# Kernel optimization log

Hardware: AMD Instinct MI355X
Metric: run time of the kernel (lower is better)

Reference implementation:

```python
import jax, jax.numpy as jnp
import numpy as np

B, N, IN_DIM, SLOT_DIM, HIDDEN = 32, 4096, 256, 256, 512
NUM_SLOTS, NUM_ITERS = 8, 3
EPS_LN = 1e-5


def layernorm(x, g, b):
    m = jnp.mean(x, axis=-1, keepdims=True)
    v = jnp.var(x, axis=-1, keepdims=True)
    return (x - m) * jax.lax.rsqrt(v + EPS_LN) * g + b


def setup_inputs() -> dict:
    key = jax.random.key(0)
    ks = jax.random.split(key, 16)
    s = 0.02
    return {
        "inputs": jax.random.normal(ks[0], (B, N, IN_DIM), jnp.float32),
        "init_noise": jax.random.normal(ks[1], (B, NUM_SLOTS, SLOT_DIM), jnp.float32),
        "mu": jax.random.normal(ks[2], (1, 1, SLOT_DIM), jnp.float32),
        "sigma_raw": jax.random.normal(ks[3], (1, 1, SLOT_DIM), jnp.float32),
        "ln_in_g": jnp.ones((IN_DIM,), jnp.float32), "ln_in_b": jnp.zeros((IN_DIM,), jnp.float32),
        "ln_s_g": jnp.ones((SLOT_DIM,), jnp.float32), "ln_s_b": jnp.zeros((SLOT_DIM,), jnp.float32),
        "ln_m_g": jnp.ones((SLOT_DIM,), jnp.float32), "ln_m_b": jnp.zeros((SLOT_DIM,), jnp.float32),
        "wq": jax.random.normal(ks[4], (SLOT_DIM, SLOT_DIM), jnp.float32) * s,
        "bq": jnp.zeros((SLOT_DIM,), jnp.float32),
        "wk": jax.random.normal(ks[5], (SLOT_DIM, IN_DIM), jnp.float32) * s,
        "bk": jnp.zeros((SLOT_DIM,), jnp.float32),
        "wv": jax.random.normal(ks[6], (SLOT_DIM, IN_DIM), jnp.float32) * s,
        "bv": jnp.zeros((SLOT_DIM,), jnp.float32),
        "w_ih": jax.random.normal(ks[7], (3 * SLOT_DIM, SLOT_DIM), jnp.float32) * s,
        "w_hh": jax.random.normal(ks[8], (3 * SLOT_DIM, SLOT_DIM), jnp.float32) * s,
        "b_ih": jnp.zeros((3 * SLOT_DIM,), jnp.float32),
        "b_hh": jnp.zeros((3 * SLOT_DIM,), jnp.float32),
        "w1": jax.random.normal(ks[9], (HIDDEN, SLOT_DIM), jnp.float32) * s,
        "b1": jnp.zeros((HIDDEN,), jnp.float32),
        "w2": jax.random.normal(ks[10], (SLOT_DIM, HIDDEN), jnp.float32) * s,
        "b2": jnp.zeros((SLOT_DIM,), jnp.float32),
    }


def gru_cell(x, h, w_ih, w_hh, b_ih, b_hh):
    # PyTorch GRUCell: gates split as (reset, update, new)
    gx = x @ w_ih.T + b_ih
    gh = h @ w_hh.T + b_hh
    xr, xz, xn = jnp.split(gx, 3, axis=-1)
    hr, hz, hn = jnp.split(gh, 3, axis=-1)
    r = jax.nn.sigmoid(xr + hr)
    z = jax.nn.sigmoid(xz + hz)
    n = jnp.tanh(xn + r * hn)
    return (1.0 - z) * n + z * h


def reference(inputs, init_noise, mu, sigma_raw, ln_in_g, ln_in_b, ln_s_g, ln_s_b,
              ln_m_g, ln_m_b, wq, bq, wk, bk, wv, bv, w_ih, w_hh, b_ih, b_hh,
              w1, b1, w2, b2):
    scale = SLOT_DIM ** (-0.5)
    x = layernorm(inputs, ln_in_g, ln_in_b)          # [B,N,Din]
    k = x @ wk.T + bk                                # [B,N,D]
    v = x @ wv.T + bv                                # [B,N,D]
    sigma = jax.nn.softplus(sigma_raw)
    slots = mu + sigma * init_noise                  # [B,S,D]
    attn = None
    for _ in range(NUM_ITERS):
        slots_prev = slots
        q = layernorm(slots, ln_s_g, ln_s_b) @ wq.T + bq      # [B,S,D]
        logits = jnp.einsum('bnd,bsd->bns', k, q) * scale     # [B,N,S]
        attn = jax.nn.softmax(logits, axis=-1) + 1e-8         # softmax over slots
        attn = attn / jnp.sum(attn, axis=1, keepdims=True)    # renorm over inputs
        updates = jnp.einsum('bnd,bns->bsd', v, attn)         # [B,S,D]
        slots = gru_cell(updates, slots_prev, w_ih, w_hh, b_ih, b_hh)
        h = jax.nn.relu(layernorm(slots, ln_m_g, ln_m_b) @ w1.T + b1)
        slots = slots + (h @ w2.T + b2)
    return slots, attn
```

## Files before the change

kernel.cpp:

```cpp
#include <hip/hip_runtime.h>
#include <hip/hip_fp16.h>
#include <cstdint>

#define DEV static __device__ __forceinline__

typedef _Float16 f16x2 __attribute__((ext_vector_type(2)));

DEV float fdot2u(uint32_t a, uint32_t b, float c){
  union U { uint32_t u; f16x2 h; };
  U ua; ua.u = a; U ub; ub.u = b;
#if __has_builtin(__builtin_amdgcn_fdot2)
  return __builtin_amdgcn_fdot2(ua.h, ub.h, c, false);
#else
  return c + (float)ua.h[0]*(float)ub.h[0] + (float)ua.h[1]*(float)ub.h[1];
#endif
}

DEV float dot4(uint4 x, uint4 w, float a){
  a = fdot2u(x.x, w.x, a); a = fdot2u(x.y, w.y, a);
  a = fdot2u(x.z, w.z, a); a = fdot2u(x.w, w.w, a);
  return a;
}

DEV float wsum64(float v){
  #pragma unroll
  for (int o = 32; o; o >>= 1) v += __shfl_xor(v, o);
  return v;
}

DEV uint32_t pack2h(float a, float b){
  __half ha = __float2half(a), hb = __float2half(b);
  return (uint32_t)__half_as_ushort(ha) | ((uint32_t)__half_as_ushort(hb) << 16);
}

DEV uint32_t packsh(float v){
  float o = __shfl_xor(v, 1);
  return pack2h(v, o);
}

DEV uint4 packrow8(const float* p){
  uint4 r;
  r.x = pack2h(p[0], p[1]); r.y = pack2h(p[2], p[3]);
  r.z = pack2h(p[4], p[5]); r.w = pack2h(p[6], p[7]);
  return r;
}

__global__ __launch_bounds__(256) void k_tr(
  const float* __restrict__ wq, const float* __restrict__ wv,
  const float* __restrict__ wih, const float* __restrict__ whh,
  const float* __restrict__ w1, const float* __restrict__ w2,
  const float* __restrict__ wk,
  uint4* __restrict__ WQp4, uint4* __restrict__ WVp4,
  uint4* __restrict__ WIHp4, uint4* __restrict__ WHHp4,
  uint4* __restrict__ W1p4, uint4* __restrict__ W2p4,
  uint4* __restrict__ WKp4)
{
  int u = blockIdx.x * 256 + threadIdx.x;
  if (u < 8192){
    int e4 = u >> 8, n = u & 255;
    WVp4[u] = packrow8(wv + n*256 + 8*e4);
  } else if (u < 32768){
    int v = u - 8192; int e4 = v / 768, n = v - e4*768;
    WIHp4[v] = packrow8(wih + n*256 + 8*e4);
  } else if (u < 57344){
    int v = u - 32768; int e4 = v / 768, n = v - e4*768;
    WHHp4[v] = packrow8(whh + n*256 + 8*e4);
  } else if (u < 73728){
    int v = u - 57344; int e4 = v >> 9, n = v & 511;
    W1p4[v] = packrow8(w1 + n*256 + 8*e4);
  } else if (u < 90112){
    int v = u - 73728; int e4 = v >> 8, n = v & 255;
    W2p4[v] = packrow8(w2 + n*512 + 8*e4);
  } else if (u < 98304){
    int v = u - 90112; int e4 = v >> 8, n = v & 255;
    WQp4[v] = packrow8(wq + n*256 + 8*e4);
  } else if (u < 106496){
    int v = u - 98304; int d4 = v >> 8, c = v & 255;
    uint4 r;
    r.x = pack2h(wk[(8*d4+0)*256 + c], wk[(8*d4+1)*256 + c]);
    r.y = pack2h(wk[(8*d4+2)*256 + c], wk[(8*d4+3)*256 + c]);
    r.z = pack2h(wk[(8*d4+4)*256 + c], wk[(8*d4+5)*256 + c]);
    r.w = pack2h(wk[(8*d4+6)*256 + c], wk[(8*d4+7)*256 + c]);
    WKp4[v] = r;
  }
}

__global__ __launch_bounds__(256) void k_ln(
  const float* __restrict__ xin, const float* __restrict__ g,
  const float* __restrict__ b, uint32_t* __restrict__ xhat)
{
  int row = blockIdx.x * 4 + (threadIdx.x >> 6);
  int lane = threadIdx.x & 63;
  const float4 xv = ((const float4*)(xin + (size_t)row * 256))[lane];
  float s1 = wsum64(xv.x + xv.y + xv.z + xv.w);
  float s2 = wsum64(xv.x*xv.x + xv.y*xv.y + xv.z*xv.z + xv.w*xv.w);
  float m = s1 * (1.0f/256.0f);
  float var = s2 * (1.0f/256.0f) - m*m;
  float rstd = rsqrtf(var + 1e-5f);
  float4 gv = ((const float4*)g)[lane];
  float4 bv = ((const float4*)b)[lane];
  float y0 = (xv.x - m)*rstd*gv.x + bv.x;
  float y1 = (xv.y - m)*rstd*gv.y + bv.y;
  float y2 = (xv.z - m)*rstd*gv.z + bv.z;
  float y3 = (xv.w - m)*rstd*gv.w + bv.w;
  ((uint2*)(xhat + (size_t)row * 128))[lane] = make_uint2(pack2h(y0,y1), pack2h(y2,y3));
}

template<int MODE>
__global__ __launch_bounds__(512) void k_slot(
  const float* __restrict__ noise, const float* __restrict__ mu,
  const float* __restrict__ sigraw, float* __restrict__ S0,
  const float* __restrict__ uacc, const float* __restrict__ asum,
  const uint4* __restrict__ WVp4, const float* __restrict__ bv,
  const uint4* __restrict__ WIHp4, const uint4* __restrict__ WHHp4,
  const float* __restrict__ bih, const float* __restrict__ bhh,
  const float* __restrict__ lmg, const float* __restrict__ lmb,
  const uint4* __restrict__ W1p4, const float* __restrict__ b1,
  const uint4* __restrict__ W2p4, const float* __restrict__ b2,
  const float* __restrict__ lsg, const float* __restrict__ lsb,
  const uint4* __restrict__ WQp4, const float* __restrict__ bq,
  const uint4* __restrict__ WKp4, const float* __restrict__ bk,
  uint32_t* __restrict__ QTH, float* __restrict__ CV,
  float* __restrict__ uacc_z, float* __restrict__ asum_z)
{
  __shared__ float gx[768], gh[768];
  __shared__ float part[512];
  __shared__ uint4 hs4[32], un4[32], us4[32], sln4[32], q4[32];
  __shared__ uint4 hb4[64];
  __shared__ float redA[8], redB[8];

  const int t = threadIdx.x;
  const int h = t >> 8;
  const int c = t & 255;
  const int lane = t & 63;
  const int w8 = t >> 6;
  const int r = blockIdx.x;
  const int b = r >> 3, s = r & 7;

  float snv = 0.f, spv = 0.f;

  if (MODE == 0){
    if (t < 256){
      float x = sigraw[c];
      float sp = (x > 20.0f) ? x : log1pf(__expf(x));
      snv = mu[c] + sp * noise[r*256 + c];
      S0[r*256 + c] = snv;
    }
  } else {
    float ainv = 1.0f / asum[r];
    float hv = 0.f;
    if (t < 256){
      hv = S0[r*256 + c];
      float unv = uacc[r*256 + c] * ainv;
      uint32_t ph = packsh(hv), pu = packsh(unv);
      if (!(c & 1)){
        ((uint32_t*)hs4)[c>>1] = ph;
        ((uint32_t*)un4)[c>>1] = pu;
      }
    }
    __syncthreads();

    {
      float a = 0.f;
      #pragma unroll 8
      for (int e4 = h*16; e4 < h*16 + 16; ++e4)
        a = dot4(un4[e4], WVp4[e4*256 + c], a);
      part[t] = a;
    }
    __syncthreads();
    if (t < 256){
      float us = part[t] + part[t + 256] + bv[c];
      uint32_t p = packsh(us);
      if (!(c & 1)) ((uint32_t*)us4)[c>>1] = p;
    }
    __syncthreads();

    {
      const uint4* IN4 = h ? hs4 : us4;
      const uint4* WP = h ? WHHp4 : WIHp4;
      float a0 = 0.f, a1 = 0.f, a2 = 0.f;
      #pragma unroll 8
      for (int e4 = 0; e4 < 32; ++e4){
        uint4 x = IN4[e4];
        a0 = dot4(x, WP[e4*768 + c], a0);
        a1 = dot4(x, WP[e4*768 + 256 + c], a1);
        a2 = dot4(x, WP[e4*768 + 512 + c], a2);
      }
      float* OUT = h ? gh : gx;
      OUT[c] = a0; OUT[256 + c] = a1; OUT[512 + c] = a2;
    }
    __syncthreads();

    if (t < 256){
      float xr = gx[c]     + bih[c];
      float xz = gx[256+c] + bih[256+c];
      float xn = gx[512+c] + bih[512+c];
      float hr = gh[c]     + bhh[c];
      float hz = gh[256+c] + bhh[256+c];
      float hn = gh[512+c] + bhh[512+c];
      float rg = 1.f/(1.f + __expf(-(xr + hr)));
      float zg = 1.f/(1.f + __expf(-(xz + hz)));
      float ng = tanhf(xn + rg*hn);
      spv = (1.f - zg)*ng + zg*hv;
      float a = wsum64(spv), bs = wsum64(spv*spv);
      if (lane == 0){ redA[w8] = a; redB[w8] = bs; }
    }
    __syncthreads();
    {
      float s1 = redA[0]+redA[1]+redA[2]+redA[3];
      float s2 = redB[0]+redB[1]+redB[2]+redB[3];
      float m = s1*(1.f/256.f), var = s2*(1.f/256.f) - m*m;
      float rstd = rsqrtf(var + 1e-5f);
      if (t < 256){
        float slv = (spv - m)*rstd*lmg[c] + lmb[c];
        uint32_t p = packsh(slv);
        if (!(c & 1)) ((uint32_t*)sln4)[c>>1] = p;
      }
    }
    __syncthreads();

    {
      float a = 0.f;
      #pragma unroll 8
      for (int e4 = 0; e4 < 32; ++e4)
        a = dot4(sln4[e4], W1p4[e4*512 + t], a);
      float hval = fmaxf(a + b1[t], 0.f);
      float o = __shfl_xor(hval, 1);
      if (!(t & 1)) ((uint32_t*)hb4)[t>>1] = pack2h(hval, o);
    }
    __syncthreads();

    {
      float a = 0.f;
      #pragma unroll 8
      for (int e4 = h*32; e4 < h*32 + 32; ++e4)
        a = dot4(hb4[e4], W2p4[e4*256 + c], a);
      part[t] = a;
    }
    __syncthreads();
    if (t < 256){
      snv = spv + part[t] + part[t + 256] + b2[c];
      S0[r*256 + c] = snv;
    }
  }

  if (MODE != 2){
    if (t < 256){
      float a = wsum64(snv), bs = wsum64(snv*snv);
      if (lane == 0){ redA[w8] = a; redB[w8] = bs; }
    }
    __syncthreads();
    {
      float s1 = redA[0]+redA[1]+redA[2]+redA[3];
      float s2 = redB[0]+redB[1]+redB[2]+redB[3];
      float m = s1*(1.f/256.f), var = s2*(1.f/256.f) - m*m;
      float rstd = rsqrtf(var + 1e-5f);
      if (t < 256){
        float slv = (snv - m)*rstd*lsg[c] + lsb[c];
        uint32_t p = packsh(slv);
        if (!(c & 1)) ((uint32_t*)sln4)[c>>1] = p;
      }
    }
    __syncthreads();

    {
      float a = 0.f;
      #pragma unroll 8
      for (int e4 = h*16; e4 < h*16 + 16; ++e4)
        a = dot4(sln4[e4], WQp4[e4*256 + c], a);
      part[t] = a;
    }
    __syncthreads();
    if (t < 256){
      float qv = part[t] + part[t + 256] + bq[c];
      float p = wsum64(bk[c] * qv);
      if (lane == 0) redA[w8] = p;
      uint32_t pk = packsh(qv);
      if (!(c & 1)) ((uint32_t*)q4)[c>>1] = pk;
    }
    __syncthreads();
    {
      float cv = redA[0]+redA[1]+redA[2]+redA[3];
      if (t == 0) CV[r] = cv;
    }

    {
      float a = 0.f;
      #pragma unroll 8
      for (int e4 = h*16; e4 < h*16 + 16; ++e4)
        a = dot4(q4[e4], WKp4[e4*256 + c], a);
      part[t] = a;
    }
    __syncthreads();
    if (t < 256){
      float qtv = part[t] + part[t + 256];
      uint32_t p = packsh(qtv);
      if (!(c & 1)) QTH[b*1024 + (c>>1)*8 + s] = p;
      uacc_z[r*256 + c] = 0.f;
    }
    if (t == 0) asum_z[r] = 0.f;
  }
}

template<bool LAST>
__global__ __launch_bounds__(256) void k_attn(
  const uint32_t* __restrict__ xhat,
  const uint32_t* __restrict__ qtpk, const float* __restrict__ cvec,
  float* __restrict__ uacc, float* __restrict__ asum,
  float* __restrict__ attn_out)
{
  __shared__ uint32_t xs[64*135];
  __shared__ float lg[64*12];
  __shared__ uint32_t qs[1024];
  __shared__ float cs[8];
  const int b = blockIdx.y, chunk = blockIdx.x;
  const int t = threadIdx.x;
  const int lane = t & 63, w = t >> 6;
  for (int i = t; i < 1024; i += 256) qs[i] = qtpk[b*1024 + i];
  if (t < 8) cs[t] = cvec[b*8 + t];
  float up[8] = {0,0,0,0,0,0,0,0};
  float asl[8] = {0,0,0,0,0,0,0,0};
  const int shf = (t & 1) * 16;
  for (int st = 0; st < 4; ++st){
    const int gr0 = b*4096 + chunk*256 + st*64;
    __syncthreads();
    #pragma unroll
    for (int k = 0; k < 8; ++k){
      int c4 = k*256 + t;
      int row = c4 >> 5, j = c4 & 31;
      uint4 dv = ((const uint4*)xhat)[(size_t)(gr0 + row)*32 + j];
      uint32_t* dst = xs + row*135 + j*4;
      dst[0] = dv.x; dst[1] = dv.y; dst[2] = dv.z; dst[3] = dv.w;
    }
    __syncthreads();
    {
      const int s0 = w*2;
      float d0 = 0.f, d1 = 0.f;
      const uint32_t* xr = xs + lane*135;
      #pragma unroll
      for (int dp = 0; dp < 128; ++dp){
        uint32_t x = xr[dp];
        uint2 q = *(const uint2*)(qs + dp*8 + s0);
        d0 = fdot2u(x, q.x, d0);
        d1 = fdot2u(x, q.y, d1);
      }
      *(float2*)(lg + lane*12 + s0) = make_float2(d0, d1);
    }
    __syncthreads();
    if (t < 64){
      float l[8];
      float4 a = *(const float4*)(lg + t*12);
      float4 b4 = *(const float4*)(lg + t*12 + 4);
      l[0]=a.x; l[1]=a.y; l[2]=a.z; l[3]=a.w;
      l[4]=b4.x; l[5]=b4.y; l[6]=b4.z; l[7]=b4.w;
      #pragma unroll
      for (int s = 0; s < 8; ++s) l[s] = (l[s] + cs[s]) * 0.0625f;
      float mx = l[0];
      #pragma unroll
      for (int s = 1; s < 8; ++s) mx = fmaxf(mx, l[s]);
      float sum = 0.f;
      #pragma unroll
      for (int s = 0; s < 8; ++s){ l[s] = __expf(l[s] - mx); sum += l[s]; }
      float inv = 1.0f / sum;
      #pragma unroll
      for (int s = 0; s < 8; ++s){ l[s] = l[s]*inv + 1e-8f; asl[s] += l[s]; }
      float4 o0 = make_float4(l[0], l[1], l[2], l[3]);
      float4 o1 = make_float4(l[4], l[5], l[6], l[7]);
      *(float4*)(lg + t*12) = o0;
      *(float4*)(lg + t*12 + 4) = o1;
      if (LAST){
        float4* ap = (float4*)(attn_out + (size_t)(gr0 + t)*8);
        ap[0] = o0; ap[1] = o1;
      }
    }
    __syncthreads();
    {
      const uint32_t* xc = xs + (t >> 1);
      #pragma unroll 8
      for (int r = 0; r < 64; ++r){
        uint32_t u = xc[r*135];
        float x = __half2float(__ushort_as_half((unsigned short)(u >> shf)));
        float4 a0 = *(const float4*)(lg + r*12);
        float4 a1 = *(const float4*)(lg + r*12 + 4);
        up[0] += a0.x*x; up[1] += a0.y*x; up[2] += a0.z*x; up[3] += a0.w*x;
        up[4] += a1.x*x; up[5] += a1.y*x; up[6] += a1.z*x; up[7] += a1.w*x;
      }
    }
  }
  #pragma unroll
  for (int s = 0; s < 8; ++s) atomicAdd(&uacc[(b*8 + s)*256 + t], up[s]);
  if (t < 64){
    #pragma unroll
    for (int s = 0; s < 8; ++s){
      float v = wsum64(asl[s]);
      if (t == 0) atomicAdd(&asum[b*8 + s], v);
    }
  }
}

__global__ __launch_bounds__(256) void k_out(
  const float* __restrict__ S0, const float* __restrict__ asum,
  float* __restrict__ out)
{
  int i = blockIdx.x * 256 + threadIdx.x;
  if (i < 65536) out[i] = S0[i];
  else {
    int j = i - 65536;
    int b = j >> 15;
    int s = j & 7;
    out[i] = out[i] * (1.0f / asum[b*8 + s]);
  }
}

extern "C" void kernel_launch(void* const* d_in, const int* in_sizes, int n_in,
                              void* d_out, int out_size, void* d_ws, size_t ws_size,
                              hipStream_t stream) {
  const float* inputs = (const float*)d_in[0];
  const float* noise  = (const float*)d_in[1];
  const float* mu     = (const float*)d_in[2];
  const float* sigraw = (const float*)d_in[3];
  const float* lng    = (const float*)d_in[4];
  const float* lnb    = (const float*)d_in[5];
  const float* lsg    = (const float*)d_in[6];
  const float* lsb    = (const float*)d_in[7];
  const float* lmg    = (const float*)d_in[8];
  const float* lmb    = (const float*)d_in[9];
  const float* wq     = (const float*)d_in[10];
  const float* bq     = (const float*)d_in[11];
  const float* wk     = (const float*)d_in[12];
  const float* bk     = (const float*)d_in[13];
  const float* wv     = (const float*)d_in[14];
  const float* bv     = (const float*)d_in[15];
  const float* wih    = (const float*)d_in[16];
  const float* whh    = (const float*)d_in[17];
  const float* bih    = (const float*)d_in[18];
  const float* bhh    = (const float*)d_in[19];
  const float* w1     = (const float*)d_in[20];
  const float* b1     = (const float*)d_in[21];
  const float* w2     = (const float*)d_in[22];
  const float* b2     = (const float*)d_in[23];
  float* out = (float*)d_out;

  char* w = (char*)d_ws;
  size_t o = 0;
  uint32_t* XH = (uint32_t*)w;  o += 67108864;
  uint32_t* QT = (uint32_t*)(w + o); o += 131072;
  float* CV  = (float*)(w + o); o += 1024;
  float* UA  = (float*)(w + o); o += 262144;
  float* AS  = (float*)(w + o); o += 1024;
  float* S0  = (float*)(w + o); o += 262144;
  uint4* WQp = (uint4*)(w + o); o += 131072;
  uint4* WVp = (uint4*)(w + o); o += 131072;
  uint4* WIHp= (uint4*)(w + o); o += 393216;
  uint4* WHHp= (uint4*)(w + o); o += 393216;
  uint4* W1p = (uint4*)(w + o); o += 262144;
  uint4* W2p = (uint4*)(w + o); o += 262144;
  uint4* WKp = (uint4*)(w + o); o += 131072;

  k_tr<<<416, 256, 0, stream>>>(wq, wv, wih, whh, w1, w2, wk,
                                WQp, WVp, WIHp, WHHp, W1p, W2p, WKp);
  k_ln<<<32768, 256, 0, stream>>>(inputs, lng, lnb, XH);
  k_slot<0><<<256, 512, 0, stream>>>(noise, mu, sigraw, S0, UA, AS,
      WVp, bv, WIHp, WHHp, bih, bhh, lmg, lmb, W1p, b1, W2p, b2,
      lsg, lsb, WQp, bq, WKp, bk, QT, CV, UA, AS);

  dim3 ga(16, 32);
  for (int it = 0; it < 3; ++it){
    if (it == 2) k_attn<true ><<<ga, 256, 0, stream>>>(XH, QT, CV, UA, AS, out + 65536);
    else         k_attn<false><<<ga, 256, 0, stream>>>(XH, QT, CV, UA, AS, out + 65536);
    if (it < 2)
      k_slot<1><<<256, 512, 0, stream>>>(noise, mu, sigraw, S0, UA, AS,
          WVp, bv, WIHp, WHHp, bih, bhh, lmg, lmb, W1p, b1, W2p, b2,
          lsg, lsb, WQp, bq, WKp, bk, QT, CV, UA, AS);
    else
      k_slot<2><<<256, 512, 0, stream>>>(noise, mu, sigraw, S0, UA, AS,
          WVp, bv, WIHp, WHHp, bih, bhh, lmg, lmb, W1p, b1, W2p, b2,
          lsg, lsb, WQp, bq, WKp, bk, QT, CV, UA, AS);
  }
  k_out<<<4352, 256, 0, stream>>>(S0, AS, out);
}
```

Baseline: 429.9 us.

## Restructure attention kernel with MFMA logits, async LDS loads and swizzled layout

Rewrites k_attn so the k·q logits are computed with 16x16x32 f16 MFMA instead of per-lane fdot2 loops, and the softmax over slots runs in all waves using lane shuffles rather than a single wave. Input tiles are now copied straight from global memory into a XOR-swizzled LDS buffer with global_load_lds, which replaces the padded register-staged copy. Each wave now handles its own 16 rows for the update accumulation, and the partial sums are reduced in LDS before the atomics. This removes the serial softmax bottleneck and the scalar dot products, at the cost of more barriers and a cross-wave reduction at the end.

```diff
diff --git a/kernel.cpp b/kernel.cpp
--- a/kernel.cpp
+++ b/kernel.cpp
@@ -5,6 +5,8 @@
 #define DEV static __device__ __forceinline__
 
 typedef _Float16 f16x2 __attribute__((ext_vector_type(2)));
+typedef _Float16 f16x8 __attribute__((ext_vector_type(8)));
+typedef float    f32x4 __attribute__((ext_vector_type(4)));
 
 DEV float fdot2u(uint32_t a, uint32_t b, float c){
   union U { uint32_t u; f16x2 h; };
@@ -43,6 +45,12 @@
   r.x = pack2h(p[0], p[1]); r.y = pack2h(p[2], p[3]);
   r.z = pack2h(p[4], p[5]); r.w = pack2h(p[6], p[7]);
   return r;
+}
+
+DEV void gld16(const void* g, void* l){
+  __builtin_amdgcn_global_load_lds(
+      (const __attribute__((address_space(1))) void*)g,
+      (__attribute__((address_space(3))) void*)l, 16, 0, 0);
 }
 
 __global__ __launch_bounds__(256) void k_tr(
@@ -309,93 +317,134 @@
   float* __restrict__ uacc, float* __restrict__ asum,
   float* __restrict__ attn_out)
 {
-  __shared__ uint32_t xs[64*135];
-  __shared__ float lg[64*12];
+  __shared__ uint32_t xs[8192];
   __shared__ uint32_t qs[1024];
-  __shared__ float cs[8];
+  __shared__ float attn_lds[64][16];
+  __shared__ float up_lds[8][256];
+
   const int b = blockIdx.y, chunk = blockIdx.x;
   const int t = threadIdx.x;
-  const int lane = t & 63, w = t >> 6;
+  const int l = t & 63, w = t >> 6;
+  const int g = l >> 4, sl = l & 15;
+
   for (int i = t; i < 1024; i += 256) qs[i] = qtpk[b*1024 + i];
-  if (t < 8) cs[t] = cvec[b*8 + t];
-  float up[8] = {0,0,0,0,0,0,0,0};
-  float asl[8] = {0,0,0,0,0,0,0,0};
-  const int shf = (t & 1) * 16;
+
+  auto stage = [&](int st){
+    const size_t gr0 = (size_t)b*4096 + (size_t)chunk*256 + st*64;
+    #pragma unroll
+    for (int i = 0; i < 8; ++i){
+      int n  = w*8 + i;
+      int rl = 2*n + (l >> 5);
+      int ql = (l & 31) ^ (rl & 7);
+      gld16(xhat + (gr0 + rl)*128 + ql*4, xs + n*256);
+    }
+  };
+
+  stage(0);
+  __syncthreads();
+
+  uint4 bq[8];
+  #pragma unroll
+  for (int kk = 0; kk < 8; ++kk){
+    if (sl < 8){
+      uint4 v;
+      v.x = qs[(16*kk + 4*g + 0)*8 + sl];
+      v.y = qs[(16*kk + 4*g + 1)*8 + sl];
+      v.z = qs[(16*kk + 4*g + 2)*8 + sl];
+      v.w = qs[(16*kk + 4*g + 3)*8 + sl];
+      bq[kk] = v;
+    } else bq[kk] = make_uint4(0u,0u,0u,0u);
+  }
+  const float cv = (sl < 8) ? cvec[b*8 + sl] : 0.f;
+
+  float up[8][4];
+  #pragma unroll
+  for (int s = 0; s < 8; ++s){ up[s][0]=0.f; up[s][1]=0.f; up[s][2]=0.f; up[s][3]=0.f; }
+  float asl_acc = 0.f;
+
   for (int st = 0; st < 4; ++st){
-    const int gr0 = b*4096 + chunk*256 + st*64;
-    __syncthreads();
+    if (st){ __syncthreads(); stage(st); __syncthreads(); }
+    const int L0 = 16*w;
+
+    f32x4 acc; acc[0]=0.f; acc[1]=0.f; acc[2]=0.f; acc[3]=0.f;
+    const int rowA = L0 + sl;
     #pragma unroll
-    for (int k = 0; k < 8; ++k){
-      int c4 = k*256 + t;
-      int row = c4 >> 5, j = c4 & 31;
-      uint4 dv = ((const uint4*)xhat)[(size_t)(gr0 + row)*32 + j];
-      uint32_t* dst = xs + row*135 + j*4;
-      dst[0] = dv.x; dst[1] = dv.y; dst[2] = dv.z; dst[3] = dv.w;
-    }
-    __syncthreads();
-    {
-      const int s0 = w*2;
-      float d0 = 0.f, d1 = 0.f;
-      const uint32_t* xr = xs + lane*135;
+    for (int kk = 0; kk < 8; ++kk){
+      uint4 av = *(const uint4*)(xs + rowA*128 + (((4*kk + g) ^ (rowA & 7)) << 2));
+      union { uint4 u; f16x8 h; } A, B;
+      A.u = av; B.u = bq[kk];
+      acc = __builtin_amdgcn_mfma_f32_16x16x32_f16(A.h, B.h, acc, 0, 0, 0);
+    }
+
+    #pragma unroll
+    for (int reg = 0; reg < 4; ++reg){
+      float d = (acc[reg] + cv) * 0.0625f;
+      float m = d;
+      m = fmaxf(m, __shfl_xor(m, 1));
+      m = fmaxf(m, __shfl_xor(m, 2));
+      m = fmaxf(m, __shfl_xor(m, 4));
+      float e = __expf(d - m);
+      float ssum = e;
+      ssum += __shfl_xor(ssum, 1);
+      ssum += __shfl_xor(ssum, 2);
+      ssum += __shfl_xor(ssum, 4);
+      float a = e / ssum + 1e-8f;
+      asl_acc += a;
+      attn_lds[L0 + 4*g + reg][sl] = a;
+    }
+
+    #pragma unroll 4
+    for (int rr = 0; rr < 16; ++rr){
+      const int row = L0 + rr;
+      const uint32_t* xp = xs + row*128 + ((((l>>1) ^ (row & 7)) << 2) | ((l & 1) << 1));
+      uint2 xv = *(const uint2*)xp;
+      float x0 = __half2float(__ushort_as_half((unsigned short)(xv.x & 0xffff)));
+      float x1 = __half2float(__ushort_as_half((unsigned short)(xv.x >> 16)));
+      float x2 = __half2float(__ushort_as_half((unsigned short)(xv.y & 0xffff)));
+      float x3 = __half2float(__ushort_as_half((unsigned short)(xv.y >> 16)));
+      const float4 a0 = *(const float4*)&attn_lds[row][0];
+      const float4 a1 = *(const float4*)&attn_lds[row][4];
+      float as8[8] = {a0.x, a0.y, a0.z, a0.w, a1.x, a1.y, a1.z, a1.w};
       #pragma unroll
-      for (int dp = 0; dp < 128; ++dp){
-        uint32_t x = xr[dp];
-        uint2 q = *(const uint2*)(qs + dp*8 + s0);
-        d0 = fdot2u(x, q.x, d0);
-        d1 = fdot2u(x, q.y, d1);
+      for (int s = 0; s < 8; ++s){
+        up[s][0] += as8[s]*x0; up[s][1] += as8[s]*x1;
+        up[s][2] += as8[s]*x2; up[s][3] += as8[s]*x3;
       }
-      *(float2*)(lg + lane*12 + s0) = make_float2(d0, d1);
-    }
-    __syncthreads();
-    if (t < 64){
-      float l[8];
-      float4 a = *(const float4*)(lg + t*12);
-      float4 b4 = *(const float4*)(lg + t*12 + 4);
-      l[0]=a.x; l[1]=a.y; l[2]=a.z; l[3]=a.w;
-      l[4]=b4.x; l[5]=b4.y; l[6]=b4.z; l[7]=b4.w;
+    }
+
+    if (LAST){
+      __syncthreads();
+      const size_t gr0 = (size_t)b*4096 + (size_t)chunk*256 + st*64;
+      int row = t >> 2, s0 = (t & 3)*2;
+      float2 v = *(const float2*)&attn_lds[row][s0];
+      *(float2*)(attn_out + (gr0 + row)*8 + s0) = v;
+    }
+  }
+
+  {
+    float v = asl_acc;
+    v += __shfl_xor(v, 16);
+    v += __shfl_xor(v, 32);
+    if (l < 8) atomicAdd(&asum[b*8 + l], v);
+  }
+
+  __syncthreads();
+  #pragma unroll
+  for (int ww = 0; ww < 4; ++ww){
+    if (w == ww){
       #pragma unroll
-      for (int s = 0; s < 8; ++s) l[s] = (l[s] + cs[s]) * 0.0625f;
-      float mx = l[0];
-      #pragma unroll
-      for (int s = 1; s < 8; ++s) mx = fmaxf(mx, l[s]);
-      float sum = 0.f;
-      #pragma unroll
-      for (int s = 0; s < 8; ++s){ l[s] = __expf(l[s] - mx); sum += l[s]; }
-      float inv = 1.0f / sum;
-      #pragma unroll
-      for (int s = 0; s < 8; ++s){ l[s] = l[s]*inv + 1e-8f; asl[s] += l[s]; }
-      float4 o0 = make_float4(l[0], l[1], l[2], l[3]);
-      float4 o1 = make_float4(l[4], l[5], l[6], l[7]);
-      *(float4*)(lg + t*12) = o0;
-      *(float4*)(lg + t*12 + 4) = o1;
-      if (LAST){
-        float4* ap = (float4*)(attn_out + (size_t)(gr0 + t)*8);
-        ap[0] = o0; ap[1] = o1;
+      for (int s = 0; s < 8; ++s){
+        float4* dst = (float4*)&up_lds[s][l*4];
+        float4 v = make_float4(up[s][0], up[s][1], up[s][2], up[s][3]);
+        if (ww){ float4 o = *dst; v.x += o.x; v.y += o.y; v.z += o.z; v.w += o.w; }
+        *dst = v;
       }
     }
     __syncthreads();
-    {
-      const uint32_t* xc = xs + (t >> 1);
-      #pragma unroll 8
-      for (int r = 0; r < 64; ++r){
-        uint32_t u = xc[r*135];
-        float x = __half2float(__ushort_as_half((unsigned short)(u >> shf)));
-        float4 a0 = *(const float4*)(lg + r*12);
-        float4 a1 = *(const float4*)(lg + r*12 + 4);
-        up[0] += a0.x*x; up[1] += a0.y*x; up[2] += a0.z*x; up[3] += a0.w*x;
-        up[4] += a1.x*x; up[5] += a1.y*x; up[6] += a1.z*x; up[7] += a1.w*x;
-      }
-    }
   }
   #pragma unroll
-  for (int s = 0; s < 8; ++s) atomicAdd(&uacc[(b*8 + s)*256 + t], up[s]);
-  if (t < 64){
-    #pragma unroll
-    for (int s = 0; s < 8; ++s){
-      float v = wsum64(asl[s]);
-      if (t == 0) atomicAdd(&asum[b*8 + s], v);
-    }
-  }
+  for (int s = 0; s < 8; ++s)
+    atomicAdd(&uacc[(b*8 + s)*256 + t], up_lds[s][t]);
 }
 
 __global__ __launch_bounds__(256) void k_out(
```

New measurement: 383.2 us. 1.12x faster.
